# Optimization experiments

Hardware: AMD Instinct MI355X
Metric: run time of the kernel (lower is better)

## Reference

```python
import jax, jax.numpy as jnp
import numpy as np

N = 50000      # nodes
E = 1250000    # edges (avg degree 32)
D = 64         # in_channels == hidden_channels
L = 3          # num_layers
IMPROVED_FILL = 2.0  # GCNConv(improved=True) self-loop weight


def setup_inputs() -> dict:
    key = jax.random.key(0)
    ks = jax.random.split(key, 6)
    x = jax.random.normal(ks[0], (N, D), dtype=jnp.float32)
    edge_index = jax.random.randint(ks[1], (2, E), 0, N, dtype=jnp.int64)
    edge_weight = jax.random.uniform(ks[2], (E,), dtype=jnp.float32)
    Ws = jax.random.normal(ks[3], (L, D, D), dtype=jnp.float32) / np.sqrt(D).astype(np.float32)
    bs = jnp.zeros((L, D), dtype=jnp.float32)
    Wf = jax.random.normal(ks[4], (D, 1), dtype=jnp.float32) / np.sqrt(D).astype(np.float32)
    bf = jnp.zeros((1,), dtype=jnp.float32)
    return dict(x=x, edge_index=edge_index, edge_weight=edge_weight,
                Ws=Ws, bs=bs, Wf=Wf, bf=bf, prob=0)


def _gcn_norm(edge_index, edge_weight, n):
    # add self-loops with fill value 2.0 (improved=True)
    loop = jnp.arange(n, dtype=edge_index.dtype)
    row = jnp.concatenate([edge_index[0], loop])  # source nodes (x_j)
    col = jnp.concatenate([edge_index[1], loop])  # target nodes (aggregation)
    w = jnp.concatenate([edge_weight,
                         jnp.full((n,), IMPROVED_FILL, edge_weight.dtype)])
    deg = jax.ops.segment_sum(w, col, num_segments=n)
    dis = jnp.where(deg > 0, jax.lax.rsqrt(deg), 0.0)  # deg^{-1/2}, inf->0
    norm = dis[row] * w * dis[col]                      # [E+N]
    return row, col, norm


def reference(x, edge_index, edge_weight, Ws, bs, Wf, bf, prob):
    n = x.shape[0]
    # gcn_norm depends only on graph structure; compute once, reuse per layer
    row, col, norm = _gcn_norm(edge_index, edge_weight, n)
    for l in range(Ws.shape[0]):
        h = x @ Ws[l]                                  # [N, D] linear transform
        msg = h[row] * norm[:, None]                   # gather + per-edge scale
        agg = jax.ops.segment_sum(msg, col, num_segments=n)  # scatter-add
        x = jax.nn.relu(agg + bs[l])
    # F.dropout(x, p=prob) with prob=0 -> identity (inference)
    return x @ Wf + bf                                 # [N, 1]
```

## Files before the change

kernel.cpp:

```cpp
#include <hip/hip_runtime.h>
#include <hip/hip_bf16.h>

#define DCH 64
#define NB_CSR 256

typedef __attribute__((ext_vector_type(8))) short bfrag;
typedef __attribute__((ext_vector_type(4))) float ffrag;

static __device__ __forceinline__ unsigned short f2bf(float f) {
    unsigned u = __float_as_uint(f);
    unsigned r = (u + 0x7fffu + ((u >> 16) & 1u)) >> 16;
    return (unsigned short)r;
}
static __device__ __forceinline__ float bf2f(unsigned short s) {
    return __uint_as_float(((unsigned)s) << 16);
}

__global__ __launch_bounds__(1024) void histrank_k(const int* __restrict__ col,
                                                   unsigned char* __restrict__ hist,
                                                   unsigned char* __restrict__ lrank,
                                                   int n, int e) {
    __shared__ unsigned bins[12544];
    int B = blockIdx.x, tid = threadIdx.x;
    int chunk = (e + NB_CSR - 1) / NB_CSR;
    int beg = B * chunk;
    int end = min(e, beg + chunk);
    int len = end - beg;
    int n4 = (n + 3) >> 2;
    for (int i = tid; i < n4; i += 1024) bins[i] = 0;
    __syncthreads();
    for (int i = tid; i < len; i += 1024) {
        int c = col[beg + i];
        unsigned sh = (c & 3) * 8;
        unsigned old = atomicAdd(&bins[c >> 2], 1u << sh);
        lrank[beg + i] = (unsigned char)((old >> sh) & 0xffu);
    }
    __syncthreads();
    unsigned* hrow32 = (unsigned*)(hist + (size_t)B * n);
    for (int i = tid; i < n4; i += 1024) hrow32[i] = bins[i];
}

__global__ __launch_bounds__(256) void hist2_k(unsigned char* __restrict__ hist,
                                               int* __restrict__ cnt, int n) {
    int g = blockIdx.x * 256 + threadIdx.x;
    int ng = n >> 2;
    if (g < ng) {
        unsigned r0 = 0, r1 = 0, r2 = 0, r3 = 0;
        size_t stride = (size_t)n >> 2;
        unsigned* p = (unsigned*)hist + g;
#pragma unroll 1
        for (int B = 0; B < NB_CSR; B += 4) {
            unsigned v0 = p[0], v1 = p[stride], v2 = p[2 * stride], v3 = p[3 * stride];
            p[0]          = (r0 & 255) | ((r1 & 255) << 8) | ((r2 & 255) << 16) | ((r3 & 255) << 24);
            r0 += v0 & 255; r1 += (v0 >> 8) & 255; r2 += (v0 >> 16) & 255; r3 += (v0 >> 24) & 255;
            p[stride]     = (r0 & 255) | ((r1 & 255) << 8) | ((r2 & 255) << 16) | ((r3 & 255) << 24);
            r0 += v1 & 255; r1 += (v1 >> 8) & 255; r2 += (v1 >> 16) & 255; r3 += (v1 >> 24) & 255;
            p[2 * stride] = (r0 & 255) | ((r1 & 255) << 8) | ((r2 & 255) << 16) | ((r3 & 255) << 24);
            r0 += v2 & 255; r1 += (v2 >> 8) & 255; r2 += (v2 >> 16) & 255; r3 += (v2 >> 24) & 255;
            p[3 * stride] = (r0 & 255) | ((r1 & 255) << 8) | ((r2 & 255) << 16) | ((r3 & 255) << 24);
            r0 += v3 & 255; r1 += (v3 >> 8) & 255; r2 += (v3 >> 16) & 255; r3 += (v3 >> 24) & 255;
            p += 4 * stride;
        }
        *(int4*)(cnt + 4 * g) = make_int4((int)r0, (int)r1, (int)r2, (int)r3);
    } else if (g == ng) {
        for (int b = ng << 2; b < n; ++b) {
            unsigned run = 0;
            for (int B = 0; B < NB_CSR; ++B) {
                unsigned char* p = hist + (size_t)B * n + b;
                unsigned v = *p; *p = (unsigned char)run; run += v;
            }
            cnt[b] = (int)run;
        }
    }
}

__global__ __launch_bounds__(1024) void scan1_k(const int* __restrict__ cnt,
                                                int* __restrict__ ptr,
                                                int* __restrict__ bsum, int n) {
    __shared__ int wtot[16];
    int tid = threadIdx.x, lane = tid & 63, w = tid >> 6;
    int i = blockIdx.x * 1024 + tid;
    int v = (i < n) ? cnt[i] : 0;
    int s = v;
#pragma unroll
    for (int off = 1; off < 64; off <<= 1) {
        int t = __shfl_up(s, off);
        if (lane >= off) s += t;
    }
    if (lane == 63) wtot[w] = s;
    __syncthreads();
    if (w == 0) {
        int t16 = (lane < 16) ? wtot[lane] : 0;
        int ss = t16;
#pragma unroll
        for (int off = 1; off < 16; off <<= 1) {
            int t = __shfl_up(ss, off);
            if (lane >= off) ss += t;
        }
        if (lane < 16) wtot[lane] = ss - t16;
    }
    __syncthreads();
    int excl = s - v + wtot[w];
    if (i < n) ptr[i] = excl;
    if (tid == 1023) bsum[blockIdx.x] = excl + v;
}

__global__ __launch_bounds__(64) void scan2_k(int* __restrict__ bsum, int nb) {
    int lane = threadIdx.x;
    int v = (lane < nb) ? bsum[lane] : 0;
    int s = v;
#pragma unroll
    for (int off = 1; off < 64; off <<= 1) {
        int t = __shfl_up(s, off);
        if (lane >= off) s += t;
    }
    if (lane < nb) bsum[lane] = s - v;
    if (lane == 63) bsum[nb] = s;
}

__global__ __launch_bounds__(1024) void scan3_k(int* __restrict__ ptr,
                                                const int* __restrict__ bsum,
                                                int n, int nb) {
    int i = blockIdx.x * 1024 + threadIdx.x;
    if (i < n) ptr[i] += bsum[blockIdx.x];
    if (i == 0) ptr[n] = bsum[nb];
}

__global__ __launch_bounds__(1024) void place_k(const int* __restrict__ row,
                                                const int* __restrict__ col,
                                                const float* __restrict__ ew,
                                                const int* __restrict__ ptr,
                                                const unsigned char* __restrict__ hist,
                                                const unsigned char* __restrict__ lrank,
                                                uint2* __restrict__ edg,
                                                int n, int e) {
    __shared__ unsigned hrow_s[12544];
    int B = blockIdx.x, tid = threadIdx.x;
    int chunk = (e + NB_CSR - 1) / NB_CSR;
    int beg = B * chunk;
    int end = min(e, beg + chunk);
    int n4 = (n + 3) >> 2;
    const unsigned* hrow32 = (const unsigned*)(hist + (size_t)B * n);
    for (int i = tid; i < n4; i += 1024) hrow_s[i] = hrow32[i];
    __syncthreads();
    const unsigned char* hrow8 = (const unsigned char*)hrow_s;
    for (int i = beg + tid; i < end; i += 1024) {
        int c = col[i];
        int p = ptr[c] + (int)hrow8[c] + (int)lrank[i];
        edg[p] = make_uint2((unsigned)row[i], __float_as_uint(ew[i]));
    }
}

__global__ __launch_bounds__(256) void deg_k(const int* __restrict__ ptr,
                                             const uint2* __restrict__ edg,
                                             float* __restrict__ dis, int n) {
    int node = blockIdx.x * 4 + (threadIdx.x >> 6);
    int lane = threadIdx.x & 63;
    if (node >= n) return;
    int beg = ptr[node], end = ptr[node + 1];
    float s = 0.f;
    for (int p = beg + lane; p < end; p += 64) s += __uint_as_float(edg[p].y);
#pragma unroll
    for (int off = 32; off > 0; off >>= 1) s += __shfl_down(s, off);
    if (lane == 0) dis[node] = rsqrtf(s + 2.0f);
}

__global__ __launch_bounds__(256) void normw_k(uint2* __restrict__ edg,
                                               const float* __restrict__ dis, int e) {
    int i = blockIdx.x * 256 + threadIdx.x;
    if (i >= e) return;
    uint2 ev = edg[i];
    ((unsigned*)edg)[2 * i + 1] =
        __float_as_uint(__uint_as_float(ev.y) * dis[ev.x]);
}

__global__ __launch_bounds__(256) void pack_k(const float* __restrict__ Ws,
                                              short* __restrict__ wpk, int L) {
    int ent = blockIdx.x * 256 + threadIdx.x;
    if (ent >= L * 512) return;
    int layer = ent >> 9;
    int r = ent & 511;
    int lane = r & 63;
    int st = r >> 6;
    int s = st >> 2, t = st & 3;
    int quad = lane >> 4;
    int ncol = t * 16 + (lane & 15);
    const float* W = Ws + (size_t)layer * DCH * DCH;
    union { short sh[8]; int4 v; } hi, lo;
#pragma unroll
    for (int j = 0; j < 8; ++j) {
        int k = s * 32 + quad * 8 + j;
        float w = W[k * DCH + ncol];
        unsigned short h = f2bf(w);
        hi.sh[j] = (short)h;
        lo.sh[j] = (short)f2bf(w - bf2f(h));
    }
    *(int4*)(wpk + ((size_t)(layer * 2 + 0) * 512 + r) * 8) = hi.v;
    *(int4*)(wpk + ((size_t)(layer * 2 + 1) * 512 + r) * 8) = lo.v;
}

__global__ __launch_bounds__(256) void gemm_k(const float* __restrict__ x,
                                              const short* __restrict__ wpk_layer,
                                              unsigned short* __restrict__ hb, int n_tiles) {
    __shared__ short Wl[2][512 * 8];
    {
        const int4* src = (const int4*)wpk_layer;
        int4* dst = (int4*)&Wl[0][0];
        for (int i = threadIdx.x; i < 1024; i += 256) dst[i] = src[i];
    }
    __syncthreads();
    int wave = threadIdx.x >> 6, lane = threadIdx.x & 63;
    int tile = blockIdx.x * 4 + wave;
    if (tile >= n_tiles) return;
    int m = lane & 15, quad = lane >> 4;
    int row = tile * 16 + m;

    float av[2][8];
    {
        const float4* p0 = (const float4*)(x + (size_t)row * DCH + quad * 8);
        const float4* p1 = (const float4*)(x + (size_t)row * DCH + 32 + quad * 8);
        float4 a0 = p0[0], a1 = p0[1], b0 = p1[0], b1 = p1[1];
        av[0][0] = a0.x; av[0][1] = a0.y; av[0][2] = a0.z; av[0][3] = a0.w;
        av[0][4] = a1.x; av[0][5] = a1.y; av[0][6] = a1.z; av[0][7] = a1.w;
        av[1][0] = b0.x; av[1][1] = b0.y; av[1][2] = b0.z; av[1][3] = b0.w;
        av[1][4] = b1.x; av[1][5] = b1.y; av[1][6] = b1.z; av[1][7] = b1.w;
    }
    bfrag ah[2], al[2];
#pragma unroll
    for (int s = 0; s < 2; ++s)
#pragma unroll
        for (int j = 0; j < 8; ++j) {
            unsigned short hbv = f2bf(av[s][j]);
            ah[s][j] = (short)hbv;
            al[s][j] = (short)f2bf(av[s][j] - bf2f(hbv));
        }

#pragma unroll
    for (int t = 0; t < 4; ++t) {
        ffrag acc = {0.f, 0.f, 0.f, 0.f};
#pragma unroll
        for (int s = 0; s < 2; ++s) {
            bfrag wh = *(bfrag*)&Wl[0][((s * 4 + t) * 64 + lane) * 8];
            bfrag wl = *(bfrag*)&Wl[1][((s * 4 + t) * 64 + lane) * 8];
            acc = __builtin_amdgcn_mfma_f32_16x16x32_bf16(ah[s], wh, acc, 0, 0, 0);
            acc = __builtin_amdgcn_mfma_f32_16x16x32_bf16(al[s], wh, acc, 0, 0, 0);
            acc = __builtin_amdgcn_mfma_f32_16x16x32_bf16(ah[s], wl, acc, 0, 0, 0);
        }
        int colc = t * 16 + m;
#pragma unroll
        for (int r = 0; r < 4; ++r)
            hb[(size_t)(tile * 16 + quad * 4 + r) * DCH + colc] = f2bf(acc[r]);
    }
}

static __device__ __forceinline__ void gather_node(int node, int lane, int p, int hf,
                                                   float dis_c,
                                                   const int* __restrict__ ptr,
                                                   const uint2* __restrict__ edg,
                                                   const unsigned* __restrict__ hbf,
                                                   float& A0, float& A1) {
    float a0 = 0.f, a1 = 0.f;
    if (hf == 0) {
        unsigned sv = hbf[(size_t)node * 32 + p];
        a0 = 2.0f * dis_c * __uint_as_float(sv << 16);
        a1 = 2.0f * dis_c * __uint_as_float(sv & 0xffff0000u);
    }
    int beg = ptr[node], end = ptr[node + 1];
    for (int base = beg; base < end; base += 64) {
        int idx = base + lane;
        int rv = 0; float nv = 0.f;
        if (idx < end) {
            uint2 ev = edg[idx];
            rv = (int)ev.x;
            nv = __uint_as_float(ev.y);
        }
        int m = min(64, end - base);
        int steps = (((m + 1) >> 1) + 7) & ~7;
        for (int j0 = 0; j0 < steps; j0 += 8) {
            unsigned hv[8]; float nn[8];
#pragma unroll
            for (int q = 0; q < 8; ++q) {
                int eidx = 2 * (j0 + q) + hf;
                int r = __shfl(rv, eidx);
                nn[q] = __shfl(nv, eidx);
                hv[q] = hbf[(size_t)r * 32 + p];
            }
#pragma unroll
            for (int q = 0; q < 8; ++q) {
                a0 += __uint_as_float(hv[q] << 16) * nn[q];
                a1 += __uint_as_float(hv[q] & 0xffff0000u) * nn[q];
            }
        }
    }
    A0 = a0 + __shfl_xor(a0, 32);
    A1 = a1 + __shfl_xor(a1, 32);
}

__global__ __launch_bounds__(256) void gg_k(const int* __restrict__ ptr,
                                            const uint2* __restrict__ edg,
                                            const float* __restrict__ dis,
                                            const unsigned* __restrict__ hbf,
                                            const float* __restrict__ b,
                                            const short* __restrict__ wpk_next,
                                            unsigned short* __restrict__ hb_out, int n) {
    __shared__ float xs[16][68];
    int w = threadIdx.x >> 6, lane = threadIdx.x & 63;
    int p = lane & 31, hf = lane >> 5;
    int tile = blockIdx.x;
    float2 bv = ((const float2*)b)[p];
#pragma unroll 1
    for (int i = 0; i < 4; ++i) {
        int node = tile * 16 + w * 4 + i;
        if (node < n) {
            float dis_c = dis[node];
            float A0, A1;
            gather_node(node, lane, p, hf, dis_c, ptr, edg, hbf, A0, A1);
            if (hf == 0) {
                xs[w * 4 + i][2 * p]     = fmaxf(dis_c * A0 + bv.x, 0.f);
                xs[w * 4 + i][2 * p + 1] = fmaxf(dis_c * A1 + bv.y, 0.f);
            }
        }
    }
    __syncthreads();
    int m = lane & 15, quad = lane >> 4, t = w;
    bfrag ah[2], al[2];
#pragma unroll
    for (int s = 0; s < 2; ++s)
#pragma unroll
        for (int j = 0; j < 8; ++j) {
            float v = xs[m][s * 32 + quad * 8 + j];
            unsigned short hbv = f2bf(v);
            ah[s][j] = (short)hbv;
            al[s][j] = (short)f2bf(v - bf2f(hbv));
        }
    ffrag acc = {0.f, 0.f, 0.f, 0.f};
#pragma unroll
    for (int s = 0; s < 2; ++s) {
        bfrag wh = *(const bfrag*)(wpk_next + ((size_t)((s * 4 + t) * 64 + lane)) * 8);
        bfrag wl = *(const bfrag*)(wpk_next + ((size_t)(512 + (s * 4 + t) * 64 + lane)) * 8);
        acc = __builtin_amdgcn_mfma_f32_16x16x32_bf16(ah[s], wh, acc, 0, 0, 0);
        acc = __builtin_amdgcn_mfma_f32_16x16x32_bf16(al[s], wh, acc, 0, 0, 0);
        acc = __builtin_amdgcn_mfma_f32_16x16x32_bf16(ah[s], wl, acc, 0, 0, 0);
    }
    int colc = t * 16 + m;
#pragma unroll
    for (int r = 0; r < 4; ++r) {
        int orow = tile * 16 + quad * 4 + r;
        if (orow < n) hb_out[(size_t)orow * DCH + colc] = f2bf(acc[r]);
    }
}

__global__ __launch_bounds__(256) void gf_k(const int* __restrict__ ptr,
                                            const uint2* __restrict__ edg,
                                            const float* __restrict__ dis,
                                            const unsigned* __restrict__ hbf,
                                            const float* __restrict__ b,
                                            const float* __restrict__ Wf,
                                            const float* __restrict__ bf,
                                            float* __restrict__ out, int n) {
    int node = blockIdx.x * 4 + (threadIdx.x >> 6);
    int lane = threadIdx.x & 63;
    if (node >= n) return;
    int p = lane & 31, hf = lane >> 5;
    float dis_c = dis[node];
    float A0, A1;
    gather_node(node, lane, p, hf, dis_c, ptr, edg, hbf, A0, A1);
    float2 bv = ((const float2*)b)[p];
    float2 wv = ((const float2*)Wf)[p];
    float x0 = fmaxf(dis_c * A0 + bv.x, 0.f);
    float x1 = fmaxf(dis_c * A1 + bv.y, 0.f);
    float v = x0 * wv.x + x1 * wv.y;
#pragma unroll
    for (int off = 16; off > 0; off >>= 1) v += __shfl_down(v, off);
    if (lane == 0) out[node] = v + bf[0];
}

extern "C" void kernel_launch(void* const* d_in, const int* in_sizes, int n_in,
                              void* d_out, int out_size, void* d_ws, size_t ws_size,
                              hipStream_t stream) {
    const float* x0 = (const float*)d_in[0];
    const int*   ei = (const int*)d_in[1];
    const float* ew = (const float*)d_in[2];
    const float* Ws = (const float*)d_in[3];
    const float* bs = (const float*)d_in[4];
    const float* Wf = (const float*)d_in[5];
    const float* bf = (const float*)d_in[6];

    const int n = in_sizes[0] / DCH;
    const int e = in_sizes[2];
    const int L = in_sizes[3] / (DCH * DCH);

    const int* row = ei;
    const int* col = ei + e;

    size_t off = 0;
    auto alloc = [&](size_t bytes) {
        off = (off + 255) & ~(size_t)255;
        void* r = (char*)d_ws + off;
        off += bytes;
        return r;
    };
    const int nb_scan = (n + 1023) / 1024;
    int*   cnt  = (int*)  alloc((size_t)n * 4);
    int*   ptr  = (int*)  alloc((size_t)(n + 1) * 4);
    int*   bsum = (int*)  alloc((size_t)(nb_scan + 1) * 4);
    float* dis  = (float*)alloc((size_t)n * 4);
    short* wpk  = (short*)alloc((size_t)L * 2 * 512 * 8 * 2);
    uint2* edg  = (uint2*)alloc((size_t)e * 8);
    unsigned char* lrank = (unsigned char*)alloc((size_t)e);
    size_t szA = (size_t)NB_CSR * n;
    size_t szH = (size_t)2 * n * DCH * 2;
    unsigned char* hist = (unsigned char*)alloc(szA > szH ? szA : szH);
    unsigned short* hb_a = (unsigned short*)hist;
    unsigned short* hb_b = hb_a + (size_t)n * DCH;

    dim3 blk(256);
    const int n_tiles = (n + 15) / 16;

    histrank_k<<<dim3(NB_CSR), dim3(1024), 0, stream>>>(col, hist, lrank, n, e);
    hist2_k   <<<dim3((n / 4 + 1 + 255) / 256), blk, 0, stream>>>(hist, cnt, n);
    scan1_k   <<<dim3(nb_scan), dim3(1024), 0, stream>>>(cnt, ptr, bsum, n);
    scan2_k   <<<dim3(1), dim3(64), 0, stream>>>(bsum, nb_scan);
    scan3_k   <<<dim3(nb_scan), dim3(1024), 0, stream>>>(ptr, bsum, n, nb_scan);
    place_k   <<<dim3(NB_CSR), dim3(1024), 0, stream>>>(row, col, ew, ptr, hist, lrank, edg, n, e);
    deg_k     <<<dim3((n + 3) / 4), blk, 0, stream>>>(ptr, edg, dis, n);
    normw_k   <<<dim3((e + 255) / 256), blk, 0, stream>>>(edg, dis, e);
    pack_k    <<<dim3((L * 512 + 255) / 256), blk, 0, stream>>>(Ws, wpk, L);

    const size_t wstride = (size_t)2 * 512 * 8;
    gemm_k<<<dim3((n_tiles + 3) / 4), blk, 0, stream>>>(x0, wpk, hb_a, n_tiles);
    gg_k  <<<dim3(n_tiles), blk, 0, stream>>>(ptr, edg, dis, (const unsigned*)hb_a,
                                              bs, wpk + wstride, hb_b, n);
    gg_k  <<<dim3(n_tiles), blk, 0, stream>>>(ptr, edg, dis, (const unsigned*)hb_b,
                                              bs + DCH, wpk + 2 * wstride, hb_a, n);
    gf_k  <<<dim3((n + 3) / 4), blk, 0, stream>>>(ptr, edg, dis, (const unsigned*)hb_a,
                                                  bs + 2 * DCH, Wf, bf, (float*)d_out, n);
}
```

Measured before the change: 254.7 us.

## Replace per-node histogram CSR build with two-level bucket sort by node bin

The CSR construction no longer uses a 256xN byte histogram, prefix scans and a rank-based placement. Instead, edges are first bucketed into coarse bins of 256 target nodes using per-block bin counts and cursors. Each bin is then sorted locally in shared memory, and the degree and rsqrt normalization are computed in that same pass. This removes the large histogram traffic, several launches, and the separate degree kernel. In exchange it adds an intermediate record buffer and packs the source index into 20 bits, which assumes n < 2^20 and at most 256 bins.

Measured after the change: 223.0 us, median of 2. -12.4%, faster.

```diff
diff --git a/kernel.cpp b/kernel.cpp
--- a/kernel.cpp
+++ b/kernel.cpp
@@ -3,6 +3,7 @@
 
 #define DCH 64
 #define NB_CSR 256
+#define MAXBINS 256
 
 typedef __attribute__((ext_vector_type(8))) short bfrag;
 typedef __attribute__((ext_vector_type(4))) float ffrag;
@@ -16,153 +17,119 @@
     return __uint_as_float(((unsigned)s) << 16);
 }
 
-__global__ __launch_bounds__(1024) void histrank_k(const int* __restrict__ col,
-                                                   unsigned char* __restrict__ hist,
-                                                   unsigned char* __restrict__ lrank,
-                                                   int n, int e) {
-    __shared__ unsigned bins[12544];
+__global__ __launch_bounds__(1024) void binc_k(const int* __restrict__ col,
+                                               unsigned* __restrict__ blkcnt, int e) {
+    __shared__ unsigned bins[MAXBINS];
     int B = blockIdx.x, tid = threadIdx.x;
     int chunk = (e + NB_CSR - 1) / NB_CSR;
-    int beg = B * chunk;
-    int end = min(e, beg + chunk);
-    int len = end - beg;
-    int n4 = (n + 3) >> 2;
-    for (int i = tid; i < n4; i += 1024) bins[i] = 0;
-    __syncthreads();
-    for (int i = tid; i < len; i += 1024) {
-        int c = col[beg + i];
-        unsigned sh = (c & 3) * 8;
-        unsigned old = atomicAdd(&bins[c >> 2], 1u << sh);
-        lrank[beg + i] = (unsigned char)((old >> sh) & 0xffu);
-    }
-    __syncthreads();
-    unsigned* hrow32 = (unsigned*)(hist + (size_t)B * n);
-    for (int i = tid; i < n4; i += 1024) hrow32[i] = bins[i];
-}
-
-__global__ __launch_bounds__(256) void hist2_k(unsigned char* __restrict__ hist,
-                                               int* __restrict__ cnt, int n) {
-    int g = blockIdx.x * 256 + threadIdx.x;
-    int ng = n >> 2;
-    if (g < ng) {
-        unsigned r0 = 0, r1 = 0, r2 = 0, r3 = 0;
-        size_t stride = (size_t)n >> 2;
-        unsigned* p = (unsigned*)hist + g;
-#pragma unroll 1
+    int beg = B * chunk, end = min(e, beg + chunk);
+    if (tid < MAXBINS) bins[tid] = 0;
+    __syncthreads();
+    for (int i = beg + tid; i < end; i += 1024)
+        atomicAdd(&bins[col[i] >> 8], 1u);
+    __syncthreads();
+    if (tid < MAXBINS) blkcnt[B * MAXBINS + tid] = bins[tid];
+}
+
+__global__ __launch_bounds__(256) void bincur_k(const unsigned* __restrict__ blkcnt,
+                                                unsigned* __restrict__ blkcur,
+                                                int* __restrict__ binbase,
+                                                int* __restrict__ ptr,
+                                                int nbins, int n, int e) {
+    __shared__ unsigned tot[MAXBINS];
+    __shared__ unsigned base[MAXBINS + 1];
+    int j = threadIdx.x;
+    unsigned t = 0;
+    if (j < nbins) {
+        for (int B = 0; B < NB_CSR; B += 8) {
+            t += blkcnt[(B + 0) * MAXBINS + j] + blkcnt[(B + 1) * MAXBINS + j]
+               + blkcnt[(B + 2) * MAXBINS + j] + blkcnt[(B + 3) * MAXBINS + j]
+               + blkcnt[(B + 4) * MAXBINS + j] + blkcnt[(B + 5) * MAXBINS + j]
+               + blkcnt[(B + 6) * MAXBINS + j] + blkcnt[(B + 7) * MAXBINS + j];
+        }
+    }
+    tot[j] = t;
+    __syncthreads();
+    if (j == 0) {
+        unsigned run = 0;
+        for (int k = 0; k < nbins; ++k) { base[k] = run; run += tot[k]; }
+        base[nbins] = run;
+    }
+    __syncthreads();
+    if (j < nbins) {
+        unsigned run = base[j];
+        binbase[j] = (int)run;
         for (int B = 0; B < NB_CSR; B += 4) {
-            unsigned v0 = p[0], v1 = p[stride], v2 = p[2 * stride], v3 = p[3 * stride];
-            p[0]          = (r0 & 255) | ((r1 & 255) << 8) | ((r2 & 255) << 16) | ((r3 & 255) << 24);
-            r0 += v0 & 255; r1 += (v0 >> 8) & 255; r2 += (v0 >> 16) & 255; r3 += (v0 >> 24) & 255;
-            p[stride]     = (r0 & 255) | ((r1 & 255) << 8) | ((r2 & 255) << 16) | ((r3 & 255) << 24);
-            r0 += v1 & 255; r1 += (v1 >> 8) & 255; r2 += (v1 >> 16) & 255; r3 += (v1 >> 24) & 255;
-            p[2 * stride] = (r0 & 255) | ((r1 & 255) << 8) | ((r2 & 255) << 16) | ((r3 & 255) << 24);
-            r0 += v2 & 255; r1 += (v2 >> 8) & 255; r2 += (v2 >> 16) & 255; r3 += (v2 >> 24) & 255;
-            p[3 * stride] = (r0 & 255) | ((r1 & 255) << 8) | ((r2 & 255) << 16) | ((r3 & 255) << 24);
-            r0 += v3 & 255; r1 += (v3 >> 8) & 255; r2 += (v3 >> 16) & 255; r3 += (v3 >> 24) & 255;
-            p += 4 * stride;
-        }
-        *(int4*)(cnt + 4 * g) = make_int4((int)r0, (int)r1, (int)r2, (int)r3);
-    } else if (g == ng) {
-        for (int b = ng << 2; b < n; ++b) {
-            unsigned run = 0;
-            for (int B = 0; B < NB_CSR; ++B) {
-                unsigned char* p = hist + (size_t)B * n + b;
-                unsigned v = *p; *p = (unsigned char)run; run += v;
-            }
-            cnt[b] = (int)run;
-        }
-    }
-}
-
-__global__ __launch_bounds__(1024) void scan1_k(const int* __restrict__ cnt,
-                                                int* __restrict__ ptr,
-                                                int* __restrict__ bsum, int n) {
-    __shared__ int wtot[16];
-    int tid = threadIdx.x, lane = tid & 63, w = tid >> 6;
-    int i = blockIdx.x * 1024 + tid;
-    int v = (i < n) ? cnt[i] : 0;
-    int s = v;
-#pragma unroll
-    for (int off = 1; off < 64; off <<= 1) {
-        int t = __shfl_up(s, off);
-        if (lane >= off) s += t;
-    }
-    if (lane == 63) wtot[w] = s;
-    __syncthreads();
-    if (w == 0) {
-        int t16 = (lane < 16) ? wtot[lane] : 0;
-        int ss = t16;
-#pragma unroll
-        for (int off = 1; off < 16; off <<= 1) {
-            int t = __shfl_up(ss, off);
-            if (lane >= off) ss += t;
-        }
-        if (lane < 16) wtot[lane] = ss - t16;
-    }
-    __syncthreads();
-    int excl = s - v + wtot[w];
-    if (i < n) ptr[i] = excl;
-    if (tid == 1023) bsum[blockIdx.x] = excl + v;
-}
-
-__global__ __launch_bounds__(64) void scan2_k(int* __restrict__ bsum, int nb) {
-    int lane = threadIdx.x;
-    int v = (lane < nb) ? bsum[lane] : 0;
-    int s = v;
-#pragma unroll
-    for (int off = 1; off < 64; off <<= 1) {
-        int t = __shfl_up(s, off);
-        if (lane >= off) s += t;
-    }
-    if (lane < nb) bsum[lane] = s - v;
-    if (lane == 63) bsum[nb] = s;
-}
-
-__global__ __launch_bounds__(1024) void scan3_k(int* __restrict__ ptr,
-                                                const int* __restrict__ bsum,
-                                                int n, int nb) {
-    int i = blockIdx.x * 1024 + threadIdx.x;
-    if (i < n) ptr[i] += bsum[blockIdx.x];
-    if (i == 0) ptr[n] = bsum[nb];
-}
-
-__global__ __launch_bounds__(1024) void place_k(const int* __restrict__ row,
-                                                const int* __restrict__ col,
-                                                const float* __restrict__ ew,
-                                                const int* __restrict__ ptr,
-                                                const unsigned char* __restrict__ hist,
-                                                const unsigned char* __restrict__ lrank,
-                                                uint2* __restrict__ edg,
-                                                int n, int e) {
-    __shared__ unsigned hrow_s[12544];
+            unsigned c0 = blkcnt[(B + 0) * MAXBINS + j];
+            unsigned c1 = blkcnt[(B + 1) * MAXBINS + j];
+            unsigned c2 = blkcnt[(B + 2) * MAXBINS + j];
+            unsigned c3 = blkcnt[(B + 3) * MAXBINS + j];
+            blkcur[(B + 0) * MAXBINS + j] = run;  run += c0;
+            blkcur[(B + 1) * MAXBINS + j] = run;  run += c1;
+            blkcur[(B + 2) * MAXBINS + j] = run;  run += c2;
+            blkcur[(B + 3) * MAXBINS + j] = run;  run += c3;
+        }
+    }
+    if (j == 0) { binbase[nbins] = e; ptr[n] = e; }
+}
+
+__global__ __launch_bounds__(1024) void binfill_k(const int* __restrict__ row,
+                                                  const int* __restrict__ col,
+                                                  const float* __restrict__ ew,
+                                                  const unsigned* __restrict__ blkcur,
+                                                  uint2* __restrict__ rec, int e) {
+    __shared__ unsigned cur[MAXBINS];
     int B = blockIdx.x, tid = threadIdx.x;
     int chunk = (e + NB_CSR - 1) / NB_CSR;
-    int beg = B * chunk;
-    int end = min(e, beg + chunk);
-    int n4 = (n + 3) >> 2;
-    const unsigned* hrow32 = (const unsigned*)(hist + (size_t)B * n);
-    for (int i = tid; i < n4; i += 1024) hrow_s[i] = hrow32[i];
-    __syncthreads();
-    const unsigned char* hrow8 = (const unsigned char*)hrow_s;
+    int beg = B * chunk, end = min(e, beg + chunk);
+    if (tid < MAXBINS) cur[tid] = blkcur[B * MAXBINS + tid];
+    __syncthreads();
     for (int i = beg + tid; i < end; i += 1024) {
         int c = col[i];
-        int p = ptr[c] + (int)hrow8[c] + (int)lrank[i];
-        edg[p] = make_uint2((unsigned)row[i], __float_as_uint(ew[i]));
-    }
-}
-
-__global__ __launch_bounds__(256) void deg_k(const int* __restrict__ ptr,
-                                             const uint2* __restrict__ edg,
-                                             float* __restrict__ dis, int n) {
-    int node = blockIdx.x * 4 + (threadIdx.x >> 6);
-    int lane = threadIdx.x & 63;
-    if (node >= n) return;
-    int beg = ptr[node], end = ptr[node + 1];
-    float s = 0.f;
-    for (int p = beg + lane; p < end; p += 64) s += __uint_as_float(edg[p].y);
-#pragma unroll
-    for (int off = 32; off > 0; off >>= 1) s += __shfl_down(s, off);
-    if (lane == 0) dis[node] = rsqrtf(s + 2.0f);
+        unsigned slot = atomicAdd(&cur[c >> 8], 1u);
+        rec[slot] = make_uint2((unsigned)row[i] | ((unsigned)(c & 255) << 20),
+                               __float_as_uint(ew[i]));
+    }
+}
+
+__global__ __launch_bounds__(1024) void csr_k(const uint2* __restrict__ rec,
+                                              const int* __restrict__ binbase,
+                                              int* __restrict__ ptr,
+                                              uint2* __restrict__ edg,
+                                              float* __restrict__ dis, int n) {
+    __shared__ unsigned ncnt[256];
+    __shared__ unsigned nbase[256];
+    __shared__ float degs[256];
+    int b = blockIdx.x, tid = threadIdx.x;
+    int beg = binbase[b], end = binbase[b + 1];
+    int node0 = b << 8;
+    int nn = min(256, n - node0);
+    if (tid < 256) { ncnt[tid] = 0; degs[tid] = 0.f; }
+    __syncthreads();
+    for (int i = beg + tid; i < end; i += 1024) {
+        uint2 r = rec[i];
+        unsigned c8 = r.x >> 20;
+        atomicAdd(&ncnt[c8], 1u);
+        atomicAdd(&degs[c8], __uint_as_float(r.y));
+    }
+    __syncthreads();
+    if (tid == 0) {
+        unsigned run = (unsigned)beg;
+        for (int k = 0; k < 256; ++k) { nbase[k] = run; run += ncnt[k]; }
+    }
+    __syncthreads();
+    if (tid < nn) {
+        ptr[node0 + tid] = (int)nbase[tid];
+        dis[node0 + tid] = rsqrtf(degs[tid] + 2.0f);
+    }
+    if (tid < 256) ncnt[tid] = 0;
+    __syncthreads();
+    for (int i = beg + tid; i < end; i += 1024) {
+        uint2 r = rec[i];
+        unsigned c8 = r.x >> 20;
+        unsigned pos = nbase[c8] + atomicAdd(&ncnt[c8], 1u);
+        edg[pos] = make_uint2(r.x & 0xFFFFFu, r.y);
+    }
 }
 
 __global__ __launch_bounds__(256) void normw_k(uint2* __restrict__ edg,
@@ -392,6 +359,7 @@
 
     const int* row = ei;
     const int* col = ei + e;
+    const int nbins = (n + 255) >> 8;
 
     size_t off = 0;
     auto alloc = [&](size_t bytes) {
@@ -400,32 +368,29 @@
         off += bytes;
         return r;
     };
-    const int nb_scan = (n + 1023) / 1024;
-    int*   cnt  = (int*)  alloc((size_t)n * 4);
-    int*   ptr  = (int*)  alloc((size_t)(n + 1) * 4);
-    int*   bsum = (int*)  alloc((size_t)(nb_scan + 1) * 4);
-    float* dis  = (float*)alloc((size_t)n * 4);
-    short* wpk  = (short*)alloc((size_t)L * 2 * 512 * 8 * 2);
-    uint2* edg  = (uint2*)alloc((size_t)e * 8);
-    unsigned char* lrank = (unsigned char*)alloc((size_t)e);
-    size_t szA = (size_t)NB_CSR * n;
+    int*      ptr     = (int*)     alloc((size_t)(n + 1) * 4);
+    float*    dis     = (float*)   alloc((size_t)n * 4);
+    short*    wpk     = (short*)   alloc((size_t)L * 2 * 512 * 8 * 2);
+    uint2*    edg     = (uint2*)   alloc((size_t)e * 8);
+    unsigned* blkcnt  = (unsigned*)alloc((size_t)NB_CSR * MAXBINS * 4);
+    unsigned* blkcur  = (unsigned*)alloc((size_t)NB_CSR * MAXBINS * 4);
+    int*      binbase = (int*)     alloc((size_t)(MAXBINS + 1) * 4);
+    size_t szR = (size_t)e * 8;
     size_t szH = (size_t)2 * n * DCH * 2;
-    unsigned char* hist = (unsigned char*)alloc(szA > szH ? szA : szH);
-    unsigned short* hb_a = (unsigned short*)hist;
+    unsigned char* regA = (unsigned char*)alloc(szR > szH ? szR : szH);
+    uint2* rec = (uint2*)regA;
+    unsigned short* hb_a = (unsigned short*)regA;
     unsigned short* hb_b = hb_a + (size_t)n * DCH;
 
     dim3 blk(256);
     const int n_tiles = (n + 15) / 16;
 
-    histrank_k<<<dim3(NB_CSR), dim3(1024), 0, stream>>>(col, hist, lrank, n, e);
-    hist2_k   <<<dim3((n / 4 + 1 + 255) / 256), blk, 0, stream>>>(hist, cnt, n);
-    scan1_k   <<<dim3(nb_scan), dim3(1024), 0, stream>>>(cnt, ptr, bsum, n);
-    scan2_k   <<<dim3(1), dim3(64), 0, stream>>>(bsum, nb_scan);
-    scan3_k   <<<dim3(nb_scan), dim3(1024), 0, stream>>>(ptr, bsum, n, nb_scan);
-    place_k   <<<dim3(NB_CSR), dim3(1024), 0, stream>>>(row, col, ew, ptr, hist, lrank, edg, n, e);
-    deg_k     <<<dim3((n + 3) / 4), blk, 0, stream>>>(ptr, edg, dis, n);
-    normw_k   <<<dim3((e + 255) / 256), blk, 0, stream>>>(edg, dis, e);
-    pack_k    <<<dim3((L * 512 + 255) / 256), blk, 0, stream>>>(Ws, wpk, L);
+    binc_k   <<<dim3(NB_CSR), dim3(1024), 0, stream>>>(col, blkcnt, e);
+    bincur_k <<<dim3(1), blk, 0, stream>>>(blkcnt, blkcur, binbase, ptr, nbins, n, e);
+    binfill_k<<<dim3(NB_CSR), dim3(1024), 0, stream>>>(row, col, ew, blkcur, rec, e);
+    csr_k    <<<dim3(nbins), dim3(1024), 0, stream>>>(rec, binbase, ptr, edg, dis, n);
+    normw_k  <<<dim3((e + 255) / 256), blk, 0, stream>>>(edg, dis, e);
+    pack_k   <<<dim3((L * 512 + 255) / 256), blk, 0, stream>>>(Ws, wpk, L);
 
     const size_t wstride = (size_t)2 * 512 * 8;
     gemm_k<<<dim3((n_tiles + 3) / 4), blk, 0, stream>>>(x0, wpk, hb_a, n_tiles);
```
